# Performance work log

Measured on AMD Instinct MI355X. Metric: run time of the kernel, lower is better.

Reference implementation:

```python
import jax, jax.numpy as jnp
import numpy as np

NUM_SKILLS = 50000
HIDDEN = 64
B, T = 8192, 1024
EPS = 1e-6


def setup_inputs() -> dict:
    key = jax.random.key(0)
    ks = jax.random.split(key, 8)
    X = jax.random.randint(ks[0], (B,), 0, NUM_SKILLS)
    y = jax.random.randint(ks[1], (B, T), 0, 2, dtype=jnp.int32)
    embed = jax.random.normal(ks[2], (NUM_SKILLS, HIDDEN), jnp.float32)
    bound = 1.0 / np.sqrt(HIDDEN)
    W0 = jax.random.uniform(ks[3], (HIDDEN, HIDDEN), jnp.float32, -bound, bound)
    b0 = jnp.zeros((HIDDEN,), jnp.float32)
    W1 = jax.random.uniform(ks[4], (HIDDEN, HIDDEN), jnp.float32, -bound, bound)
    b1 = jnp.zeros((HIDDEN,), jnp.float32)
    Wout = jax.random.uniform(ks[5], (HIDDEN, 4), jnp.float32, -bound, bound)
    bout = jnp.zeros((4,), jnp.float32)
    return {"X": X, "y": y, "embed": embed, "W0": W0, "b0": b0,
            "W1": W1, "b1": b1, "Wout": Wout, "bout": bout}


def reference(X, y, embed, W0, b0, W1, b1, Wout, bout):
    # Per-student BKT params from embedding + 2-layer MLP + sigmoid, clamped
    h = embed[X]                                   # (B, H)
    h = jax.nn.relu(h @ W0 + b0)
    h = jax.nn.relu(h @ W1 + b1)
    params = jnp.clip(jax.nn.sigmoid(h @ Wout + bout), EPS, 1.0 - EPS)  # (B, 4)
    l, g, s, prior = params[:, 0], params[:, 1], params[:, 2], params[:, 3]

    def step(latent, y_t):
        true_correct = jnp.where(y_t == -1, 0, y_t)
        correct = latent * (1.0 - s) + (1.0 - latent) * g
        k_t1 = latent * (1.0 - s) / correct
        k_t0 = latent * s / (latent * s + (1.0 - latent) * (1.0 - g))
        k_t = jnp.where(true_correct > 0.5, k_t1, k_t0)
        next_latent = jnp.clip(k_t + (1.0 - k_t) * l, EPS, 1.0 - EPS)
        return next_latent, (correct, latent)

    _, (corrects, latents) = jax.lax.scan(step, prior, y.T)  # scan over T
    return corrects.T, latents.T                            # (B, T) each
```

## Files before the change

### kernel.cpp

```cpp
#include <hip/hip_runtime.h>

#define TSTEPS 1024
#define NROWS  8192
#define NCHUNK 16
#define CLEN   64
#define KEPS   1e-6f

__global__ __launch_bounds__(64) void bkt_fused(
    const int* __restrict__ X, const int* __restrict__ y,
    const float* __restrict__ embed,
    const float* __restrict__ W0, const float* __restrict__ b0,
    const float* __restrict__ W1, const float* __restrict__ b1,
    const float* __restrict__ Wout, const float* __restrict__ bout,
    float* __restrict__ out_corr, float* __restrict__ out_lat)
{
    const int lane    = threadIdx.x;
    const int rowbase = blockIdx.x * 4;

    __shared__ float sh[4][64];

    #pragma unroll
    for (int rs = 0; rs < 4; ++rs) {
        const int skill = X[rowbase + rs];
        sh[rs][lane] = embed[(size_t)skill * 64 + lane];
    }
    __syncthreads();

    float a0 = b0[lane], a1 = a0, a2 = a0, a3 = a0;
    #pragma unroll
    for (int k4 = 0; k4 < 16; ++k4) {
        const float4 e0 = *(const float4*)&sh[0][k4 * 4];
        const float4 e1 = *(const float4*)&sh[1][k4 * 4];
        const float4 e2 = *(const float4*)&sh[2][k4 * 4];
        const float4 e3 = *(const float4*)&sh[3][k4 * 4];
        const float w0 = W0[(k4 * 4 + 0) * 64 + lane];
        const float w1 = W0[(k4 * 4 + 1) * 64 + lane];
        const float w2 = W0[(k4 * 4 + 2) * 64 + lane];
        const float w3 = W0[(k4 * 4 + 3) * 64 + lane];
        a0 = fmaf(e0.x, w0, a0); a0 = fmaf(e0.y, w1, a0); a0 = fmaf(e0.z, w2, a0); a0 = fmaf(e0.w, w3, a0);
        a1 = fmaf(e1.x, w0, a1); a1 = fmaf(e1.y, w1, a1); a1 = fmaf(e1.z, w2, a1); a1 = fmaf(e1.w, w3, a1);
        a2 = fmaf(e2.x, w0, a2); a2 = fmaf(e2.y, w1, a2); a2 = fmaf(e2.z, w2, a2); a2 = fmaf(e2.w, w3, a2);
        a3 = fmaf(e3.x, w0, a3); a3 = fmaf(e3.y, w1, a3); a3 = fmaf(e3.z, w2, a3); a3 = fmaf(e3.w, w3, a3);
    }
    __syncthreads();
    sh[0][lane] = fmaxf(a0, 0.f);
    sh[1][lane] = fmaxf(a1, 0.f);
    sh[2][lane] = fmaxf(a2, 0.f);
    sh[3][lane] = fmaxf(a3, 0.f);
    __syncthreads();

    a0 = b1[lane]; a1 = a0; a2 = a0; a3 = a0;
    #pragma unroll
    for (int k4 = 0; k4 < 16; ++k4) {
        const float4 e0 = *(const float4*)&sh[0][k4 * 4];
        const float4 e1 = *(const float4*)&sh[1][k4 * 4];
        const float4 e2 = *(const float4*)&sh[2][k4 * 4];
        const float4 e3 = *(const float4*)&sh[3][k4 * 4];
        const float w0 = W1[(k4 * 4 + 0) * 64 + lane];
        const float w1 = W1[(k4 * 4 + 1) * 64 + lane];
        const float w2 = W1[(k4 * 4 + 2) * 64 + lane];
        const float w3 = W1[(k4 * 4 + 3) * 64 + lane];
        a0 = fmaf(e0.x, w0, a0); a0 = fmaf(e0.y, w1, a0); a0 = fmaf(e0.z, w2, a0); a0 = fmaf(e0.w, w3, a0);
        a1 = fmaf(e1.x, w0, a1); a1 = fmaf(e1.y, w1, a1); a1 = fmaf(e1.z, w2, a1); a1 = fmaf(e1.w, w3, a1);
        a2 = fmaf(e2.x, w0, a2); a2 = fmaf(e2.y, w1, a2); a2 = fmaf(e2.z, w2, a2); a2 = fmaf(e2.w, w3, a2);
        a3 = fmaf(e3.x, w0, a3); a3 = fmaf(e3.y, w1, a3); a3 = fmaf(e3.z, w2, a3); a3 = fmaf(e3.w, w3, a3);
    }
    const float h0r = fmaxf(a0, 0.f), h1r = fmaxf(a1, 0.f);
    const float h2r = fmaxf(a2, 0.f), h3r = fmaxf(a3, 0.f);

    const float4 wo = ((const float4*)Wout)[lane];
    float p[4][4];
    p[0][0] = h0r * wo.x; p[0][1] = h0r * wo.y; p[0][2] = h0r * wo.z; p[0][3] = h0r * wo.w;
    p[1][0] = h1r * wo.x; p[1][1] = h1r * wo.y; p[1][2] = h1r * wo.z; p[1][3] = h1r * wo.w;
    p[2][0] = h2r * wo.x; p[2][1] = h2r * wo.y; p[2][2] = h2r * wo.z; p[2][3] = h2r * wo.w;
    p[3][0] = h3r * wo.x; p[3][1] = h3r * wo.y; p[3][2] = h3r * wo.z; p[3][3] = h3r * wo.w;
    #pragma unroll
    for (int off = 32; off >= 1; off >>= 1) {
        #pragma unroll
        for (int rs = 0; rs < 4; ++rs)
            #pragma unroll
            for (int c = 0; c < 4; ++c)
                p[rs][c] += __shfl_xor(p[rs][c], off, 64);
    }
    const float4 bo = *(const float4*)bout;

    const int rsme = lane >> 4;
    const int cme  = lane & 15;
    float v0 = (rsme == 0) ? p[0][0] : (rsme == 1) ? p[1][0] : (rsme == 2) ? p[2][0] : p[3][0];
    float v1 = (rsme == 0) ? p[0][1] : (rsme == 1) ? p[1][1] : (rsme == 2) ? p[2][1] : p[3][1];
    float v2 = (rsme == 0) ? p[0][2] : (rsme == 1) ? p[1][2] : (rsme == 2) ? p[2][2] : p[3][2];
    float v3 = (rsme == 0) ? p[0][3] : (rsme == 1) ? p[1][3] : (rsme == 2) ? p[2][3] : p[3][3];
    v0 += bo.x; v1 += bo.y; v2 += bo.z; v3 += bo.w;

    const float l     = fminf(fmaxf(1.0f / (1.0f + __expf(-v0)), KEPS), 1.0f - KEPS);
    const float g     = fminf(fmaxf(1.0f / (1.0f + __expf(-v1)), KEPS), 1.0f - KEPS);
    const float s     = fminf(fmaxf(1.0f / (1.0f + __expf(-v2)), KEPS), 1.0f - KEPS);
    const float prior = fminf(fmaxf(1.0f / (1.0f + __expf(-v3)), KEPS), 1.0f - KEPS);

    unsigned long long mask = 0ull;
    #pragma unroll
    for (int rs = 0; rs < 4; ++rs) {
        #pragma unroll
        for (int c = 0; c < 16; ++c) {
            const int val = y[(size_t)(rowbase + rs) * TSTEPS + c * CLEN + lane];
            const unsigned long long bal = __ballot(val > 0);
            if (lane == rs * 16 + c) mask = bal;
        }
    }

    const float c1 = 1.f - s - g, d1 = g;
    const float e00_1 = fmaf(l, c1, (1.f - l) * (1.f - s));
    const float e01_1 = l * d1;
    const float c0 = s + g - 1.f, d0 = 1.f - g;
    const float e00_0 = fmaf(l, c0, (1.f - l) * s);
    const float e01_0 = l * d0;

    float m00 = 1.f, m01 = 0.f, m10 = 0.f, m11 = 1.f;
    #pragma unroll
    for (int tt = 0; tt < CLEN; ++tt) {
        const bool one = (mask >> tt) & 1ull;
        const float e00 = one ? e00_1 : e00_0;
        const float e01 = one ? e01_1 : e01_0;
        const float e10 = one ? c1 : c0;
        const float e11 = one ? d1 : d0;
        float n00 = fmaf(e00, m00, e01 * m10);
        float n01 = fmaf(e00, m01, e01 * m11);
        float n10 = fmaf(e10, m00, e11 * m10);
        float n11 = fmaf(e10, m01, e11 * m11);
        if ((tt & 3) == 3) {
            const float inv = __builtin_amdgcn_rcpf(n11);
            m00 = n00 * inv; m01 = n01 * inv; m10 = n10 * inv; m11 = 1.f;
        } else {
            m00 = n00; m01 = n01; m10 = n10; m11 = n11;
        }
    }

    const int grp = lane & 48;
    float L  = prior;
    float L0 = prior;
    #pragma unroll
    for (int cc = 0; cc < 16; ++cc) {
        const float q00 = __shfl(m00, grp | cc, 64);
        const float q01 = __shfl(m01, grp | cc, 64);
        const float q10 = __shfl(m10, grp | cc, 64);
        const float q11 = __shfl(m11, grp | cc, 64);
        if (cme == cc) L0 = L;
        const float num = fmaf(q00, L, q01);
        const float den = fmaf(q10, L, q11);
        L = num * __builtin_amdgcn_rcpf(den);
        L = fminf(fmaxf(L, KEPS), 1.f - KEPS);
    }

    const float a    = 1.f - s;
    const float c1v  = a - g;
    const float omg  = 1.f - g;
    const float c2v  = s - omg;
    const float oml  = 1.f - l;

    const size_t obase = (size_t)(rowbase + rsme) * TSTEPS + cme * CLEN;
    float Lc = L0;
    #pragma unroll
    for (int w = 0; w < 4; ++w) {
        float cr[4], lt[4];
        #pragma unroll
        for (int q = 0; q < 16; ++q) {
            const int tt = w * 16 + q;
            const float correct = fmaf(Lc, c1v, g);
            const float den0    = fmaf(Lc, c2v, omg);
            const float k1 = (Lc * a) * __builtin_amdgcn_rcpf(correct);
            const float k0 = (Lc * s) * __builtin_amdgcn_rcpf(den0);
            const bool one = (mask >> tt) & 1ull;
            const float k = one ? k1 : k0;
            cr[q & 3] = correct;
            lt[q & 3] = Lc;
            Lc = fminf(fmaxf(fmaf(k, oml, l), KEPS), 1.f - KEPS);
            if ((q & 3) == 3) {
                const size_t o = obase + w * 16 + (q - 3);
                *(float4*)&out_corr[o] = make_float4(cr[0], cr[1], cr[2], cr[3]);
                *(float4*)&out_lat [o] = make_float4(lt[0], lt[1], lt[2], lt[3]);
            }
        }
    }
}

extern "C" void kernel_launch(void* const* d_in, const int* in_sizes, int n_in,
                              void* d_out, int out_size, void* d_ws, size_t ws_size,
                              hipStream_t stream) {
    const int*   X     = (const int*)  d_in[0];
    const int*   y     = (const int*)  d_in[1];
    const float* embed = (const float*)d_in[2];
    const float* W0    = (const float*)d_in[3];
    const float* b0    = (const float*)d_in[4];
    const float* W1    = (const float*)d_in[5];
    const float* b1    = (const float*)d_in[6];
    const float* Wout  = (const float*)d_in[7];
    const float* bout  = (const float*)d_in[8];

    float* out_corr = (float*)d_out;
    float* out_lat  = out_corr + (size_t)NROWS * TSTEPS;

    bkt_fused<<<NROWS / 4, 64, 0, stream>>>(X, y, embed, W0, b0, W1, b1, Wout, bout,
                                            out_corr, out_lat);
}
```

Baseline: 136.3 us.

## Split MLP and scan into two kernels, one row per wavefront with shuffle prefix scan

Separates the per-student parameter MLP into its own kernel that writes params to workspace. The scan kernel then gives each wavefront one row, with each lane holding 16 contiguous timesteps loaded as int4. This replaces the ballot-based mask build and the 16-step serial chunk combine with a log-depth shfl_up scan over 2x2 Möbius matrices. The aim is to cut the serial latency chain and the y-load inefficiency, at the cost of an extra launch and a workspace round trip.

```diff
diff --git a/kernel.cpp b/kernel.cpp
--- a/kernel.cpp
+++ b/kernel.cpp
@@ -2,37 +2,44 @@
 
 #define TSTEPS 1024
 #define NROWS  8192
-#define NCHUNK 16
-#define CLEN   64
+#define CLEN   16
 #define KEPS   1e-6f
 
-__global__ __launch_bounds__(64) void bkt_fused(
-    const int* __restrict__ X, const int* __restrict__ y,
-    const float* __restrict__ embed,
+__device__ __forceinline__ float clampP(float x) {
+    return fminf(fmaxf(x, KEPS), 1.f - KEPS);
+}
+__device__ __forceinline__ float sigm(float v) {
+    return 1.0f / (1.0f + __expf(-v));
+}
+
+__global__ __launch_bounds__(256) void bkt_params_v4(
+    const int* __restrict__ X, const float* __restrict__ embed,
     const float* __restrict__ W0, const float* __restrict__ b0,
     const float* __restrict__ W1, const float* __restrict__ b1,
     const float* __restrict__ Wout, const float* __restrict__ bout,
-    float* __restrict__ out_corr, float* __restrict__ out_lat)
+    float4* __restrict__ params)
 {
-    const int lane    = threadIdx.x;
-    const int rowbase = blockIdx.x * 4;
-
-    __shared__ float sh[4][64];
+    const int lane    = threadIdx.x & 63;
+    const int wid     = threadIdx.x >> 6;
+    const int rowbase = blockIdx.x * 16 + wid * 4;
+
+    __shared__ float sh[4][4][64];
+    float (*shw)[64] = sh[wid];
 
     #pragma unroll
     for (int rs = 0; rs < 4; ++rs) {
         const int skill = X[rowbase + rs];
-        sh[rs][lane] = embed[(size_t)skill * 64 + lane];
+        shw[rs][lane] = embed[(size_t)skill * 64 + lane];
     }
     __syncthreads();
 
     float a0 = b0[lane], a1 = a0, a2 = a0, a3 = a0;
     #pragma unroll
     for (int k4 = 0; k4 < 16; ++k4) {
-        const float4 e0 = *(const float4*)&sh[0][k4 * 4];
-        const float4 e1 = *(const float4*)&sh[1][k4 * 4];
-        const float4 e2 = *(const float4*)&sh[2][k4 * 4];
-        const float4 e3 = *(const float4*)&sh[3][k4 * 4];
+        const float4 e0 = *(const float4*)&shw[0][k4 * 4];
+        const float4 e1 = *(const float4*)&shw[1][k4 * 4];
+        const float4 e2 = *(const float4*)&shw[2][k4 * 4];
+        const float4 e3 = *(const float4*)&shw[3][k4 * 4];
         const float w0 = W0[(k4 * 4 + 0) * 64 + lane];
         const float w1 = W0[(k4 * 4 + 1) * 64 + lane];
         const float w2 = W0[(k4 * 4 + 2) * 64 + lane];
@@ -43,19 +50,19 @@
         a3 = fmaf(e3.x, w0, a3); a3 = fmaf(e3.y, w1, a3); a3 = fmaf(e3.z, w2, a3); a3 = fmaf(e3.w, w3, a3);
     }
     __syncthreads();
-    sh[0][lane] = fmaxf(a0, 0.f);
-    sh[1][lane] = fmaxf(a1, 0.f);
-    sh[2][lane] = fmaxf(a2, 0.f);
-    sh[3][lane] = fmaxf(a3, 0.f);
+    shw[0][lane] = fmaxf(a0, 0.f);
+    shw[1][lane] = fmaxf(a1, 0.f);
+    shw[2][lane] = fmaxf(a2, 0.f);
+    shw[3][lane] = fmaxf(a3, 0.f);
     __syncthreads();
 
     a0 = b1[lane]; a1 = a0; a2 = a0; a3 = a0;
     #pragma unroll
     for (int k4 = 0; k4 < 16; ++k4) {
-        const float4 e0 = *(const float4*)&sh[0][k4 * 4];
-        const float4 e1 = *(const float4*)&sh[1][k4 * 4];
-        const float4 e2 = *(const float4*)&sh[2][k4 * 4];
-        const float4 e3 = *(const float4*)&sh[3][k4 * 4];
+        const float4 e0 = *(const float4*)&shw[0][k4 * 4];
+        const float4 e1 = *(const float4*)&shw[1][k4 * 4];
+        const float4 e2 = *(const float4*)&shw[2][k4 * 4];
+        const float4 e3 = *(const float4*)&shw[3][k4 * 4];
         const float w0 = W1[(k4 * 4 + 0) * 64 + lane];
         const float w1 = W1[(k4 * 4 + 1) * 64 + lane];
         const float w2 = W1[(k4 * 4 + 2) * 64 + lane];
@@ -83,30 +90,41 @@
                 p[rs][c] += __shfl_xor(p[rs][c], off, 64);
     }
     const float4 bo = *(const float4*)bout;
-
-    const int rsme = lane >> 4;
-    const int cme  = lane & 15;
-    float v0 = (rsme == 0) ? p[0][0] : (rsme == 1) ? p[1][0] : (rsme == 2) ? p[2][0] : p[3][0];
-    float v1 = (rsme == 0) ? p[0][1] : (rsme == 1) ? p[1][1] : (rsme == 2) ? p[2][1] : p[3][1];
-    float v2 = (rsme == 0) ? p[0][2] : (rsme == 1) ? p[1][2] : (rsme == 2) ? p[2][2] : p[3][2];
-    float v3 = (rsme == 0) ? p[0][3] : (rsme == 1) ? p[1][3] : (rsme == 2) ? p[2][3] : p[3][3];
-    v0 += bo.x; v1 += bo.y; v2 += bo.z; v3 += bo.w;
-
-    const float l     = fminf(fmaxf(1.0f / (1.0f + __expf(-v0)), KEPS), 1.0f - KEPS);
-    const float g     = fminf(fmaxf(1.0f / (1.0f + __expf(-v1)), KEPS), 1.0f - KEPS);
-    const float s     = fminf(fmaxf(1.0f / (1.0f + __expf(-v2)), KEPS), 1.0f - KEPS);
-    const float prior = fminf(fmaxf(1.0f / (1.0f + __expf(-v3)), KEPS), 1.0f - KEPS);
-
-    unsigned long long mask = 0ull;
-    #pragma unroll
-    for (int rs = 0; rs < 4; ++rs) {
-        #pragma unroll
-        for (int c = 0; c < 16; ++c) {
-            const int val = y[(size_t)(rowbase + rs) * TSTEPS + c * CLEN + lane];
-            const unsigned long long bal = __ballot(val > 0);
-            if (lane == rs * 16 + c) mask = bal;
-        }
-    }
+    float v0 = (lane == 0) ? p[0][0] : (lane == 1) ? p[1][0] : (lane == 2) ? p[2][0] : p[3][0];
+    float v1 = (lane == 0) ? p[0][1] : (lane == 1) ? p[1][1] : (lane == 2) ? p[2][1] : p[3][1];
+    float v2 = (lane == 0) ? p[0][2] : (lane == 1) ? p[1][2] : (lane == 2) ? p[2][2] : p[3][2];
+    float v3 = (lane == 0) ? p[0][3] : (lane == 1) ? p[1][3] : (lane == 2) ? p[2][3] : p[3][3];
+    if (lane < 4) {
+        float4 r;
+        r.x = clampP(sigm(v0 + bo.x));
+        r.y = clampP(sigm(v1 + bo.y));
+        r.z = clampP(sigm(v2 + bo.z));
+        r.w = clampP(sigm(v3 + bo.w));
+        params[rowbase + lane] = r;
+    }
+}
+
+__global__ __launch_bounds__(256) void bkt_scan_v4(
+    const int* __restrict__ y, const float4* __restrict__ params,
+    float* __restrict__ out_corr, float* __restrict__ out_lat)
+{
+    const int lane = threadIdx.x & 63;
+    const int row  = blockIdx.x * 4 + (threadIdx.x >> 6);
+
+    const float4 p = params[row];
+    const float l = p.x, g = p.y, s = p.z, prior = p.w;
+
+    const int4* yb = (const int4*)(y + (size_t)row * TSTEPS + lane * CLEN);
+    const int4 v0 = yb[0], v1 = yb[1], v2 = yb[2], v3 = yb[3];
+    unsigned msk = 0;
+    msk |= (v0.x > 0) ? 1u << 0  : 0u; msk |= (v0.y > 0) ? 1u << 1  : 0u;
+    msk |= (v0.z > 0) ? 1u << 2  : 0u; msk |= (v0.w > 0) ? 1u << 3  : 0u;
+    msk |= (v1.x > 0) ? 1u << 4  : 0u; msk |= (v1.y > 0) ? 1u << 5  : 0u;
+    msk |= (v1.z > 0) ? 1u << 6  : 0u; msk |= (v1.w > 0) ? 1u << 7  : 0u;
+    msk |= (v2.x > 0) ? 1u << 8  : 0u; msk |= (v2.y > 0) ? 1u << 9  : 0u;
+    msk |= (v2.z > 0) ? 1u << 10 : 0u; msk |= (v2.w > 0) ? 1u << 11 : 0u;
+    msk |= (v3.x > 0) ? 1u << 12 : 0u; msk |= (v3.y > 0) ? 1u << 13 : 0u;
+    msk |= (v3.z > 0) ? 1u << 14 : 0u; msk |= (v3.w > 0) ? 1u << 15 : 0u;
 
     const float c1 = 1.f - s - g, d1 = g;
     const float e00_1 = fmaf(l, c1, (1.f - l) * (1.f - s));
@@ -117,17 +135,17 @@
 
     float m00 = 1.f, m01 = 0.f, m10 = 0.f, m11 = 1.f;
     #pragma unroll
-    for (int tt = 0; tt < CLEN; ++tt) {
-        const bool one = (mask >> tt) & 1ull;
+    for (int t = 0; t < CLEN; ++t) {
+        const bool one = (msk >> t) & 1u;
         const float e00 = one ? e00_1 : e00_0;
         const float e01 = one ? e01_1 : e01_0;
         const float e10 = one ? c1 : c0;
         const float e11 = one ? d1 : d0;
-        float n00 = fmaf(e00, m00, e01 * m10);
-        float n01 = fmaf(e00, m01, e01 * m11);
-        float n10 = fmaf(e10, m00, e11 * m10);
-        float n11 = fmaf(e10, m01, e11 * m11);
-        if ((tt & 3) == 3) {
+        const float n00 = fmaf(e00, m00, e01 * m10);
+        const float n01 = fmaf(e00, m01, e01 * m11);
+        const float n10 = fmaf(e10, m00, e11 * m10);
+        const float n11 = fmaf(e10, m01, e11 * m11);
+        if ((t & 3) == 3) {
             const float inv = __builtin_amdgcn_rcpf(n11);
             m00 = n00 * inv; m01 = n01 * inv; m10 = n10 * inv; m11 = 1.f;
         } else {
@@ -135,51 +153,59 @@
         }
     }
 
-    const int grp = lane & 48;
-    float L  = prior;
-    float L0 = prior;
-    #pragma unroll
-    for (int cc = 0; cc < 16; ++cc) {
-        const float q00 = __shfl(m00, grp | cc, 64);
-        const float q01 = __shfl(m01, grp | cc, 64);
-        const float q10 = __shfl(m10, grp | cc, 64);
-        const float q11 = __shfl(m11, grp | cc, 64);
-        if (cme == cc) L0 = L;
-        const float num = fmaf(q00, L, q01);
-        const float den = fmaf(q10, L, q11);
-        L = num * __builtin_amdgcn_rcpf(den);
-        L = fminf(fmaxf(L, KEPS), 1.f - KEPS);
-    }
-
-    const float a    = 1.f - s;
-    const float c1v  = a - g;
-    const float omg  = 1.f - g;
-    const float c2v  = s - omg;
-    const float oml  = 1.f - l;
-
-    const size_t obase = (size_t)(rowbase + rsme) * TSTEPS + cme * CLEN;
+    float s00 = m00, s01 = m01, s10 = m10, s11 = m11;
+    #pragma unroll
+    for (int d = 1; d < 64; d <<= 1) {
+        const float t00 = __shfl_up(s00, d, 64);
+        const float t01 = __shfl_up(s01, d, 64);
+        const float t10 = __shfl_up(s10, d, 64);
+        const float t11 = __shfl_up(s11, d, 64);
+        if (lane >= d) {
+            const float r00 = fmaf(s00, t00, s01 * t10);
+            const float r01 = fmaf(s00, t01, s01 * t11);
+            const float r10 = fmaf(s10, t00, s11 * t10);
+            const float r11 = fmaf(s10, t01, s11 * t11);
+            const float inv = __builtin_amdgcn_rcpf(r11);
+            s00 = r00 * inv; s01 = r01 * inv; s10 = r10 * inv; s11 = 1.f;
+        }
+    }
+    const float x00 = __shfl_up(s00, 1, 64);
+    const float x01 = __shfl_up(s01, 1, 64);
+    const float x10 = __shfl_up(s10, 1, 64);
+    const float x11 = __shfl_up(s11, 1, 64);
+    float L0;
+    if (lane == 0) {
+        L0 = prior;
+    } else {
+        const float num = fmaf(x00, prior, x01);
+        const float den = fmaf(x10, prior, x11);
+        L0 = clampP(num * __builtin_amdgcn_rcpf(den));
+    }
+
+    const float a   = 1.f - s;
+    const float omg = 1.f - g;
+    const float oml = 1.f - l;
+    float* oc = out_corr + (size_t)row * TSTEPS + lane * CLEN;
+    float* ol = out_lat  + (size_t)row * TSTEPS + lane * CLEN;
     float Lc = L0;
     #pragma unroll
     for (int w = 0; w < 4; ++w) {
         float cr[4], lt[4];
         #pragma unroll
-        for (int q = 0; q < 16; ++q) {
-            const int tt = w * 16 + q;
-            const float correct = fmaf(Lc, c1v, g);
-            const float den0    = fmaf(Lc, c2v, omg);
+        for (int q = 0; q < 4; ++q) {
+            const int t = w * 4 + q;
+            const float correct = fmaf(Lc, c1, g);
+            const float den0    = fmaf(Lc, c0, omg);
             const float k1 = (Lc * a) * __builtin_amdgcn_rcpf(correct);
             const float k0 = (Lc * s) * __builtin_amdgcn_rcpf(den0);
-            const bool one = (mask >> tt) & 1ull;
+            const bool one = (msk >> t) & 1u;
             const float k = one ? k1 : k0;
-            cr[q & 3] = correct;
-            lt[q & 3] = Lc;
-            Lc = fminf(fmaxf(fmaf(k, oml, l), KEPS), 1.f - KEPS);
-            if ((q & 3) == 3) {
-                const size_t o = obase + w * 16 + (q - 3);
-                *(float4*)&out_corr[o] = make_float4(cr[0], cr[1], cr[2], cr[3]);
-                *(float4*)&out_lat [o] = make_float4(lt[0], lt[1], lt[2], lt[3]);
-            }
+            cr[q] = correct;
+            lt[q] = Lc;
+            Lc = clampP(fmaf(k, oml, l));
         }
+        *(float4*)(oc + w * 4) = make_float4(cr[0], cr[1], cr[2], cr[3]);
+        *(float4*)(ol + w * 4) = make_float4(lt[0], lt[1], lt[2], lt[3]);
     }
 }
 
@@ -198,7 +224,8 @@
 
     float* out_corr = (float*)d_out;
     float* out_lat  = out_corr + (size_t)NROWS * TSTEPS;
-
-    bkt_fused<<<NROWS / 4, 64, 0, stream>>>(X, y, embed, W0, b0, W1, b1, Wout, bout,
-                                            out_corr, out_lat);
-}
+    float4* paramsb = (float4*)d_ws;
+
+    bkt_params_v4<<<NROWS / 16, 256, 0, stream>>>(X, embed, W0, b0, W1, b1, Wout, bout, paramsb);
+    bkt_scan_v4 <<<NROWS / 4,  256, 0, stream>>>(y, paramsb, out_corr, out_lat);
+}
```

Measured after the change: 132.6 us. -2.6%, faster.
